# Performance work log

Hardware: AMD Instinct MI355X
Metric: run time of the kernel (lower is better)

## Reference

```python
import jax, jax.numpy as jnp
import numpy as np

MODES1, MODES2 = 32, 32

def fht_matrix(N):
    # Exact linear-operator form of the repo's recursive fht1d (N must be a power of two,
    # which it is here, so the pad/truncate branch never triggers).
    if N == 1:
        return np.ones((1, 1), np.float32)
    M = fht_matrix(N // 2)
    k = np.arange(N // 2)
    cas = (np.cos(2 * np.pi * k / N) + np.sin(2 * np.pi * k / N)).astype(np.float32)[:, None]
    E = np.zeros((N // 2, N), np.float32); E[:, 0::2] = M   # even-index sub-transform
    O = np.zeros((N // 2, N), np.float32); O[:, 1::2] = M   # odd-index sub-transform
    return np.concatenate([E + cas * O, E - cas * O], axis=0)

def dht2(x, M1, M2):
    # apply the (pseudo-)Hartley transform along dims 2 then 3: X[k,l] = sum_{h,w} M1[k,h] M2[l,w] x[h,w]
    return jnp.einsum('bchw,kh,lw->bckl', x, M1, M2)

def neg_freq(a):
    # index map k -> (-k mod m) on the last two dims (flip then roll by 1)
    return jnp.roll(jnp.flip(a, axis=(-2, -1)), shift=(1, 1), axis=(-2, -1))

def compl_mul2d(x1, x2):
    x1n = neg_freq(x1)
    x2n = neg_freq(x2)
    return 0.5 * (jnp.einsum('bixy,ioxy->boxy', x1, x2)
                  - jnp.einsum('bixy,ioxy->boxy', x1n, x2n)
                  + jnp.einsum('bixy,ioxy->boxy', x1, x2n)
                  + jnp.einsum('bixy,ioxy->boxy', x1n, x2))

def setup_inputs() -> dict:
    key = jax.random.key(0)
    k1, k2 = jax.random.split(key)
    B, Cin, Cout, S = 32, 64, 64, 128
    x = jax.random.normal(k1, (B, Cin, S, S), jnp.float32)
    scale = 1.0 / (Cin * Cout)
    weights1 = scale * jax.random.uniform(k2, (Cin, Cout, MODES1, MODES2), jnp.float32)
    return {"x": x, "weights1": weights1}

def reference(x, weights1):
    B, Cin, S1, S2 = x.shape
    Cout = weights1.shape[1]
    M1 = jnp.asarray(fht_matrix(S1))
    M2 = jnp.asarray(fht_matrix(S2))
    x_ht = dht2(x, M1, M2)                                        # [B,Cin,S1,S2]
    block = compl_mul2d(x_ht[:, :, :MODES1, :MODES2], weights1)   # [B,Cout,m1,m2]
    out_ht = jnp.zeros((B, Cout, S1, S2), x.dtype).at[:, :, :MODES1, :MODES2].set(block)
    # idht = dht / (S1*S2)
    return dht2(out_ht, M1, M2) / (S1 * S2)
```

## Files before the change

kernel.cpp:

```cpp
#include <hip/hip_runtime.h>
#include <math.h>


#define SS   128
#define MD   32
#define NBAT 32
#define CI   64
#define CO   64

#define TWO_PI 6.2831853071795864769

typedef __attribute__((ext_vector_type(8))) short bf16x8;
typedef __attribute__((ext_vector_type(4))) float f32x4;

static const size_t OFF_M    = 0;
static const size_t OFF_MT   = 16384;
static const size_t OFF_XH   = 32768;
static const size_t OFF_XHT  = 32768 + 2097152;
static const size_t OFF_WT   = 32768 + 2 * 2097152;
static const size_t OFF_BLKT = OFF_XH;
static const size_t OFF_BLK  = OFF_XHT;
static const size_t OFF_MFH  = OFF_WT + 4194304;
static const size_t OFF_MFL  = OFF_MFH + 2048;

__device__ inline float m_entry(int k, int n) {
    float prod = 1.f;
    int kk = k, nn = n;
    for (int Nj = SS; Nj > 1; Nj >>= 1) {
        int half = Nj >> 1;
        int k1 = kk & (half - 1);
        if (nn & 1) {
            double ang = (TWO_PI / (double)Nj) * (double)k1;
            float cas = (float)(cos(ang) + sin(ang));
            prod *= (kk < half) ? cas : -cas;
        }
        kk = k1;
        nn >>= 1;
    }
    return prod;
}

__device__ inline unsigned short f2bf(float f) {
    unsigned u = __float_as_uint(f);
    return (unsigned short)((u + 0x7FFF + ((u >> 16) & 1)) >> 16);
}
__device__ inline float bf2f(unsigned short h) {
    return __uint_as_float((unsigned)h << 16);
}
__device__ inline void split2(float a, float b, unsigned& hi, unsigned& lo) {
    unsigned short ah = f2bf(a), bh = f2bf(b);
    hi = (unsigned)ah | ((unsigned)bh << 16);
    lo = (unsigned)f2bf(a - bf2f(ah)) | ((unsigned)f2bf(b - bf2f(bh)) << 16);
}

__global__ __launch_bounds__(256) void k_prep(const float* __restrict__ wgt,
                                              float* __restrict__ M,
                                              float* __restrict__ MT,
                                              float* __restrict__ Wt,
                                              unsigned short* __restrict__ MFH,
                                              unsigned short* __restrict__ MFL) {
    const int bid = blockIdx.x;
    const int t   = threadIdx.x;
    if (bid < 64) {
        int idx = bid * 256 + t;
        int k = idx >> 7, n = idx & 127;
        float prod = m_entry(k, n);
        M[idx] = prod;
        MT[n * 128 + k] = prod;
        return;
    }
    if (bid >= 4160) {
        int idx2 = (bid - 4160) * 256 + t;
        int j    = idx2 & 7;
        int lane = (idx2 >> 3) & 63;
        int s    = (idx2 >> 9) & 3;
        int tt   = idx2 >> 11;
        int kq   = tt * 16 + (lane & 15);
        int nq   = s * 32 + ((lane >> 4) << 3) + j;
        float f  = m_entry(kq, nq);
        unsigned short hi = f2bf(f);
        MFH[idx2] = hi;
        MFL[idx2] = f2bf(f - bf2f(hi));
        return;
    }
    __shared__ float tile[32][33];
    const int b2  = bid - 64;
    const int mt  = b2 & 31;
    const int iot = b2 >> 5;
    const int tx = t & 31;
    const int ty = t >> 5;
#pragma unroll
    for (int j = 0; j < 4; ++j) {
        int r = ty + 8 * j;
        tile[r][tx] = wgt[(iot * 32 + r) * 1024 + mt * 32 + tx];
    }
    __syncthreads();
#pragma unroll
    for (int j = 0; j < 4; ++j) {
        int r = ty + 8 * j;
        Wt[(mt * 32 + r) * 4096 + iot * 32 + tx] = tile[tx][r];
    }
}

__global__ __launch_bounds__(256, 3) void k_fwd2(const float* __restrict__ x,
                                                 const unsigned short* __restrict__ MFH,
                                                 const unsigned short* __restrict__ MFL,
                                                 float* __restrict__ Xh) {
    const int bc = blockIdx.x;
    const float* xp = x + (size_t)bc * 16384;
    const int t = threadIdx.x;
    const int lane = t & 63, wid = t >> 6;
    const int l15 = lane & 15, g = lane >> 4;

    __shared__ unsigned short Pan[2][2][4096];
    __shared__ unsigned short Ybf[2][32 * 136];

    const int sh0 = t >> 3, swq = t & 7;

    {
#pragma unroll
        for (int q = 0; q < 4; ++q) {
            int h = sh0 + 32 * q;
            float4 v = *(const float4*)(xp + h * 128 + swq * 4);
            unsigned h01, l01, h23, l23;
            split2(v.x, v.y, h01, l01);
            split2(v.z, v.w, h23, l23);
            int i8 = h * 8 + (swq ^ ((h & 3) << 1));
            ((uint2*)&Pan[0][0][0])[i8] = make_uint2(h01, h23);
            ((uint2*)&Pan[0][1][0])[i8] = make_uint2(l01, l23);
        }
    }

    f32x4 acc[2][2] = {};
    const int hbase = wid * 32;

    for (int s = 0; s < 4; ++s) {
        __syncthreads();
        const int cur = s & 1, nxt = cur ^ 1;
        float4 pre[4];
        if (s < 3) {
#pragma unroll
            for (int q = 0; q < 4; ++q)
                pre[q] = *(const float4*)(xp + (sh0 + 32 * q) * 128 + (s + 1) * 32 + swq * 4);
        }
        bf16x8 Bh[2], Bl[2];
#pragma unroll
        for (int lt = 0; lt < 2; ++lt) {
            int bidx = (lt * 4 + s) * 64 + lane;
            Bh[lt] = ((const bf16x8*)MFH)[bidx];
            Bl[lt] = ((const bf16x8*)MFL)[bidx];
        }
#pragma unroll
        for (int hh = 0; hh < 2; ++hh) {
            int h = hbase + hh * 16 + l15;
            int aidx = h * 4 + (g ^ (h & 3));
            bf16x8 Ah = ((const bf16x8*)&Pan[cur][0][0])[aidx];
            bf16x8 Al = ((const bf16x8*)&Pan[cur][1][0])[aidx];
#pragma unroll
            for (int lt = 0; lt < 2; ++lt) {
                acc[hh][lt] = __builtin_amdgcn_mfma_f32_16x16x32_bf16(Ah, Bh[lt], acc[hh][lt], 0, 0, 0);
                acc[hh][lt] = __builtin_amdgcn_mfma_f32_16x16x32_bf16(Ah, Bl[lt], acc[hh][lt], 0, 0, 0);
                acc[hh][lt] = __builtin_amdgcn_mfma_f32_16x16x32_bf16(Al, Bh[lt], acc[hh][lt], 0, 0, 0);
            }
        }
        if (s < 3) {
#pragma unroll
            for (int q = 0; q < 4; ++q) {
                int h = sh0 + 32 * q;
                unsigned h01, l01, h23, l23;
                split2(pre[q].x, pre[q].y, h01, l01);
                split2(pre[q].z, pre[q].w, h23, l23);
                int i8 = h * 8 + (swq ^ ((h & 3) << 1));
                ((uint2*)&Pan[nxt][0][0])[i8] = make_uint2(h01, h23);
                ((uint2*)&Pan[nxt][1][0])[i8] = make_uint2(l01, l23);
            }
        }
    }

#pragma unroll
    for (int hh = 0; hh < 2; ++hh) {
#pragma unroll
        for (int lt = 0; lt < 2; ++lt) {
            int lmode = lt * 16 + l15;
            int h0 = hbase + hh * 16 + g * 4;
            f32x4 v = acc[hh][lt];
            unsigned hi01, lo01, hi23, lo23;
            split2(v[0], v[1], hi01, lo01);
            split2(v[2], v[3], hi23, lo23);
            ((uint2*)&Ybf[0][0])[lmode * 34 + (h0 >> 2)] = make_uint2(hi01, hi23);
            ((uint2*)&Ybf[1][0])[lmode * 34 + (h0 >> 2)] = make_uint2(lo01, lo23);
        }
    }
    __syncthreads();

    const int kt = wid >> 1, lt2 = wid & 1;
    f32x4 z = {};
#pragma unroll
    for (int s2 = 0; s2 < 4; ++s2) {
        int aidx = (kt * 4 + s2) * 64 + lane;
        bf16x8 Ah = ((const bf16x8*)MFH)[aidx];
        bf16x8 Al = ((const bf16x8*)MFL)[aidx];
        int lmode = lt2 * 16 + l15;
        int yidx = lmode * 17 + s2 * 4 + g;
        bf16x8 Yh = ((const bf16x8*)&Ybf[0][0])[yidx];
        bf16x8 Yl = ((const bf16x8*)&Ybf[1][0])[yidx];
        z = __builtin_amdgcn_mfma_f32_16x16x32_bf16(Ah, Yh, z, 0, 0, 0);
        z = __builtin_amdgcn_mfma_f32_16x16x32_bf16(Ah, Yl, z, 0, 0, 0);
        z = __builtin_amdgcn_mfma_f32_16x16x32_bf16(Al, Yh, z, 0, 0, 0);
    }
    float* op = Xh + (size_t)bc * 1024;
#pragma unroll
    for (int r = 0; r < 4; ++r)
        op[(kt * 16 + g * 4 + r) * 32 + lt2 * 16 + l15] = z[r];
}

__global__ __launch_bounds__(256) void t_xh(const float* __restrict__ Xh,
                                            float* __restrict__ Xh_t) {
    __shared__ float tile[32][33];
    const int i  = blockIdx.x & 63;
    const int mt = blockIdx.x >> 6;
    const int tx = threadIdx.x & 31;
    const int ty = threadIdx.x >> 5;
#pragma unroll
    for (int j = 0; j < 4; ++j) {
        int b = ty + 8 * j;
        tile[b][tx] = Xh[(b * 64 + i) * 1024 + mt * 32 + tx];
    }
    __syncthreads();
#pragma unroll
    for (int j = 0; j < 4; ++j) {
        int row = ty + 8 * j;
        Xh_t[(mt * 32 + row) * 2048 + i * 32 + tx] = tile[tx][row];
    }
}

__global__ __launch_bounds__(256) void k_mix4(const float* __restrict__ Xh_t,
                                              const float* __restrict__ Wt,
                                              float* __restrict__ blk_t) {
    const int m  = blockIdx.x;
    const int xm = m >> 5, ym = m & 31;
    const int nm = (((32 - xm) & 31) << 5) | ((32 - ym) & 31);
    if (m > nm) return;
    const int t = threadIdx.x;

    __shared__ float Xs[2][64][32];

    {
        const float4* xm4 = (const float4*)(Xh_t + m * 2048);
        const float4* xn4 = (const float4*)(Xh_t + nm * 2048);
        float4* s0 = (float4*)&Xs[0][0][0];
        float4* s1 = (float4*)&Xs[1][0][0];
        s0[t]       = xm4[t];
        s0[t + 256] = xm4[t + 256];
        s1[t]       = xn4[t];
        s1[t + 256] = xn4[t + 256];
    }
    __syncthreads();

    const int o  = t & 63;
    const int bq = t >> 6;
    const float* wpm = Wt + m * 4096 + o;
    const float* wpn = Wt + nm * 4096 + o;

    float am[8], an[8];
#pragma unroll
    for (int j = 0; j < 8; ++j) { am[j] = 0.f; an[j] = 0.f; }

#pragma unroll 4
    for (int i = 0; i < 64; ++i) {
        float wm = wpm[i * 64];
        float wn = wpn[i * 64];
        float we = 0.5f * (wm + wn);
        float wo = 0.5f * (wm - wn);
        const float* xr  = &Xs[0][i][bq * 8];
        const float* xrn = &Xs[1][i][bq * 8];
#pragma unroll
        for (int j = 0; j < 8; ++j) {
            float x1  = xr[j];
            float x1n = xrn[j];
            am[j] = fmaf(x1, we, fmaf(x1n, wo, am[j]));
            an[j] = fmaf(x1n, we, fmaf(x1, -wo, an[j]));
        }
    }

    float* om = blk_t + m * 2048 + o;
    float* on = blk_t + nm * 2048 + o;
#pragma unroll
    for (int j = 0; j < 8; ++j) {
        int b = bq * 8 + j;
        om[b * 64] = am[j];
        on[b * 64] = an[j];
    }
}

__global__ __launch_bounds__(256) void t_blk(const float* __restrict__ blk_t,
                                             float* __restrict__ blk) {
    __shared__ float tile[32][33];
    const int mt  = blockIdx.x & 31;
    const int bot = blockIdx.x >> 5;
    const int tx = threadIdx.x & 31;
    const int ty = threadIdx.x >> 5;
#pragma unroll
    for (int j = 0; j < 4; ++j) {
        int r = ty + 8 * j;
        tile[r][tx] = blk_t[(mt * 32 + r) * 2048 + bot * 32 + tx];
    }
    __syncthreads();
#pragma unroll
    for (int j = 0; j < 4; ++j) {
        int r = ty + 8 * j;
        blk[(bot * 32 + r) * 1024 + mt * 32 + tx] = tile[tx][r];
    }
}

__global__ __launch_bounds__(256) void k_inv(const float* __restrict__ blk,
                                             const float* __restrict__ M,
                                             const float* __restrict__ MT,
                                             float* __restrict__ out) {
    const int bo = blockIdx.x;
    const int t  = threadIdx.x;
    __shared__ float smem[8448];
    float* Mcs  = smem;
    float* Ts   = smem + 4224;
    float* outS = smem;

#pragma unroll
    for (int j = 0; j < 16; ++j) {
        int idx = t + j * 256;
        int r = idx >> 5, h = idx & 31;
        Mcs[r * 33 + h] = M[r * 128 + h] * (1.f / 16384.f);
    }
    __syncthreads();

    const int r  = t & 127;
    const int rh = __builtin_amdgcn_readfirstlane(t >> 7);

    {
        const float* bp = blk + (size_t)bo * (MD * MD);
        float acc[16];
#pragma unroll
        for (int j = 0; j < 16; ++j) acc[j] = 0.f;
#pragma unroll 4
        for (int h = 0; h < MD; ++h) {
            float mc = Mcs[r * 33 + h];
            const float* brow = bp + h * MD + rh * 16;
#pragma unroll
            for (int j = 0; j < 16; ++j)
                acc[j] = fmaf(brow[j], mc, acc[j]);
        }
#pragma unroll
        for (int j = 0; j < 16; ++j) Ts[r * 33 + rh * 16 + j] = acc[j];
    }
    __syncthreads();

    float acc[64];
#pragma unroll
    for (int j = 0; j < 64; ++j) acc[j] = 0.f;
#pragma unroll 2
    for (int l = 0; l < MD; ++l) {
        float tv = Ts[r * 33 + l];
        const float* mt = MT + l * 128 + rh * 64;
#pragma unroll
        for (int j = 0; j < 64; ++j)
            acc[j] = fmaf(mt[j], tv, acc[j]);
    }

    float* op = out + (size_t)bo * (SS * SS);
    for (int rr = 0; rr < 2; ++rr) {
        __syncthreads();
        if (rh == rr) {
#pragma unroll
            for (int j = 0; j < 64; ++j) outS[r * 65 + j] = acc[j];
        }
        __syncthreads();
        const int cc = t & 63;
        const int r0 = t >> 6;
#pragma unroll
        for (int j = 0; j < 32; ++j) {
            int rrow = r0 + 4 * j;
            op[rrow * SS + rr * 64 + cc] = outS[rrow * 65 + cc];
        }
    }
}

extern "C" void kernel_launch(void* const* d_in, const int* in_sizes, int n_in,
                              void* d_out, int out_size, void* d_ws, size_t ws_size,
                              hipStream_t stream) {
    const float* x   = (const float*)d_in[0];
    const float* wgt = (const float*)d_in[1];
    float* outp = (float*)d_out;
    float* ws   = (float*)d_ws;

    float* M     = ws + OFF_M;
    float* MT    = ws + OFF_MT;
    float* Xh    = ws + OFF_XH;
    float* Xh_t  = ws + OFF_XHT;
    float* Wt    = ws + OFF_WT;
    float* blk_t = ws + OFF_BLKT;
    float* blk   = ws + OFF_BLK;
    unsigned short* MFH = (unsigned short*)(ws + OFF_MFH);
    unsigned short* MFL = (unsigned short*)(ws + OFF_MFL);

    k_prep <<<4176, 256, 0, stream>>>(wgt, M, MT, Wt, MFH, MFL);
    k_fwd2 <<<2048, 256, 0, stream>>>(x, MFH, MFL, Xh);
    t_xh   <<<2048, 256, 0, stream>>>(Xh, Xh_t);
    k_mix4 <<<1024, 256, 0, stream>>>(Xh_t, Wt, blk_t);
    t_blk  <<<2048, 256, 0, stream>>>(blk_t, blk);
    k_inv  <<<2048, 256, 0, stream>>>(blk, M, MT, outp);
}
```

Measured before the change: 122.4 us.

## Rewrite inverse Hartley transform with split-bf16 MFMA and drop fp32 matrix prep

Replaces the scalar-FMA inverse transform kernel with one that runs both separable matrix products on bf16 MFMA instructions. It uses hi/lo bf16 splitting and three MFMAs per tile to keep near-fp32 accuracy. The intermediate is staged in LDS as split bf16, and results are written with float4 stores. The fp32 M/MT precompute in the prep kernel is removed, and the inverse now reuses the packed MFH/MFL fragments also used by the forward kernel. This cuts FMA and VGPR pressure in the largest output-writing kernel, at the cost of extra rounding from the bf16 split.

```diff
diff --git a/kernel.cpp b/kernel.cpp
--- a/kernel.cpp
+++ b/kernel.cpp
@@ -13,15 +13,13 @@
 typedef __attribute__((ext_vector_type(8))) short bf16x8;
 typedef __attribute__((ext_vector_type(4))) float f32x4;
 
-static const size_t OFF_M    = 0;
-static const size_t OFF_MT   = 16384;
 static const size_t OFF_XH   = 32768;
 static const size_t OFF_XHT  = 32768 + 2097152;
 static const size_t OFF_WT   = 32768 + 2 * 2097152;
 static const size_t OFF_BLKT = OFF_XH;
 static const size_t OFF_BLK  = OFF_XHT;
 static const size_t OFF_MFH  = OFF_WT + 4194304;
-static const size_t OFF_MFL  = OFF_MFH + 2048;
+static const size_t OFF_MFL  = OFF_MFH + 8192;
 
 __device__ inline float m_entry(int k, int n) {
     float prod = 1.f;
@@ -54,23 +52,13 @@
 }
 
 __global__ __launch_bounds__(256) void k_prep(const float* __restrict__ wgt,
-                                              float* __restrict__ M,
-                                              float* __restrict__ MT,
                                               float* __restrict__ Wt,
                                               unsigned short* __restrict__ MFH,
                                               unsigned short* __restrict__ MFL) {
     const int bid = blockIdx.x;
     const int t   = threadIdx.x;
-    if (bid < 64) {
-        int idx = bid * 256 + t;
-        int k = idx >> 7, n = idx & 127;
-        float prod = m_entry(k, n);
-        M[idx] = prod;
-        MT[n * 128 + k] = prod;
-        return;
-    }
-    if (bid >= 4160) {
-        int idx2 = (bid - 4160) * 256 + t;
+    if (bid >= 4096) {
+        int idx2 = (bid - 4096) * 256 + t;
         int j    = idx2 & 7;
         int lane = (idx2 >> 3) & 63;
         int s    = (idx2 >> 9) & 3;
@@ -84,9 +72,8 @@
         return;
     }
     __shared__ float tile[32][33];
-    const int b2  = bid - 64;
-    const int mt  = b2 & 31;
-    const int iot = b2 >> 5;
+    const int mt  = bid & 31;
+    const int iot = bid >> 5;
     const int tx = t & 31;
     const int ty = t >> 5;
 #pragma unroll
@@ -313,72 +300,76 @@
     }
 }
 
-__global__ __launch_bounds__(256) void k_inv(const float* __restrict__ blk,
-                                             const float* __restrict__ M,
-                                             const float* __restrict__ MT,
-                                             float* __restrict__ out) {
+__global__ __launch_bounds__(256, 2) void k_inv2(const float* __restrict__ blk,
+                                                 const unsigned short* __restrict__ MFH,
+                                                 const unsigned short* __restrict__ MFL,
+                                                 float* __restrict__ out) {
     const int bo = blockIdx.x;
     const int t  = threadIdx.x;
-    __shared__ float smem[8448];
-    float* Mcs  = smem;
-    float* Ts   = smem + 4224;
-    float* outS = smem;
-
-#pragma unroll
-    for (int j = 0; j < 16; ++j) {
-        int idx = t + j * 256;
-        int r = idx >> 5, h = idx & 31;
-        Mcs[r * 33 + h] = M[r * 128 + h] * (1.f / 16384.f);
-    }
-    __syncthreads();
-
-    const int r  = t & 127;
-    const int rh = __builtin_amdgcn_readfirstlane(t >> 7);
+    const int lane = t & 63, wid = t >> 6;
+    const int l15 = lane & 15, g = lane >> 4;
+
+    __shared__ __align__(16) unsigned short Bst[2][32 * 40];
+    __shared__ __align__(16) unsigned short Tl[2][128 * 40];
 
     {
-        const float* bp = blk + (size_t)bo * (MD * MD);
-        float acc[16];
-#pragma unroll
-        for (int j = 0; j < 16; ++j) acc[j] = 0.f;
-#pragma unroll 4
-        for (int h = 0; h < MD; ++h) {
-            float mc = Mcs[r * 33 + h];
-            const float* brow = bp + h * MD + rh * 16;
-#pragma unroll
-            for (int j = 0; j < 16; ++j)
-                acc[j] = fmaf(brow[j], mc, acc[j]);
-        }
-#pragma unroll
-        for (int j = 0; j < 16; ++j) Ts[r * 33 + rh * 16 + j] = acc[j];
-    }
-    __syncthreads();
-
-    float acc[64];
-#pragma unroll
-    for (int j = 0; j < 64; ++j) acc[j] = 0.f;
-#pragma unroll 2
-    for (int l = 0; l < MD; ++l) {
-        float tv = Ts[r * 33 + l];
-        const float* mt = MT + l * 128 + rh * 64;
-#pragma unroll
-        for (int j = 0; j < 64; ++j)
-            acc[j] = fmaf(mt[j], tv, acc[j]);
-    }
+        float4 v = ((const float4*)(blk + (size_t)bo * 1024))[t];
+        const int h = t >> 3, l0 = (t & 7) * 4;
+        float vv[4] = { v.x * (1.f / 16384.f), v.y * (1.f / 16384.f),
+                        v.z * (1.f / 16384.f), v.w * (1.f / 16384.f) };
+#pragma unroll
+        for (int q = 0; q < 4; ++q) {
+            unsigned short hi = f2bf(vv[q]);
+            Bst[0][(l0 + q) * 40 + h] = hi;
+            Bst[1][(l0 + q) * 40 + h] = f2bf(vv[q] - bf2f(hi));
+        }
+    }
+    __syncthreads();
+
+#pragma unroll
+    for (int rr = 0; rr < 2; ++rr) {
+        const int tt = wid * 2 + rr;
+        const int aidx = (tt * 4) * 64 + lane;
+        bf16x8 Ah = ((const bf16x8*)MFH)[aidx];
+        bf16x8 Al = ((const bf16x8*)MFL)[aidx];
+#pragma unroll
+        for (int lt = 0; lt < 2; ++lt) {
+            bf16x8 Bh = *(const bf16x8*)&Bst[0][(lt * 16 + l15) * 40 + g * 8];
+            bf16x8 Bl = *(const bf16x8*)&Bst[1][(lt * 16 + l15) * 40 + g * 8];
+            f32x4 acc = {};
+            acc = __builtin_amdgcn_mfma_f32_16x16x32_bf16(Ah, Bh, acc, 0, 0, 0);
+            acc = __builtin_amdgcn_mfma_f32_16x16x32_bf16(Al, Bh, acc, 0, 0, 0);
+            acc = __builtin_amdgcn_mfma_f32_16x16x32_bf16(Ah, Bl, acc, 0, 0, 0);
+#pragma unroll
+            for (int ri = 0; ri < 4; ++ri) {
+                int r = tt * 16 + g * 4 + ri;
+                int l = lt * 16 + l15;
+                unsigned short hi = f2bf(acc[ri]);
+                Tl[0][r * 40 + l] = hi;
+                Tl[1][r * 40 + l] = f2bf(acc[ri] - bf2f(hi));
+            }
+        }
+    }
+    __syncthreads();
 
     float* op = out + (size_t)bo * (SS * SS);
+#pragma unroll
     for (int rr = 0; rr < 2; ++rr) {
-        __syncthreads();
-        if (rh == rr) {
-#pragma unroll
-            for (int j = 0; j < 64; ++j) outS[r * 65 + j] = acc[j];
-        }
-        __syncthreads();
-        const int cc = t & 63;
-        const int r0 = t >> 6;
-#pragma unroll
-        for (int j = 0; j < 32; ++j) {
-            int rrow = r0 + 4 * j;
-            op[rrow * SS + rr * 64 + cc] = outS[rrow * 65 + cc];
+        const int rt = wid * 2 + rr;
+        bf16x8 Bh = *(const bf16x8*)&Tl[0][(rt * 16 + l15) * 40 + g * 8];
+        bf16x8 Bl = *(const bf16x8*)&Tl[1][(rt * 16 + l15) * 40 + g * 8];
+        const int r = rt * 16 + l15;
+#pragma unroll
+        for (int ct = 0; ct < 8; ++ct) {
+            const int aidx = (ct * 4) * 64 + lane;
+            bf16x8 Ah = ((const bf16x8*)MFH)[aidx];
+            bf16x8 Al = ((const bf16x8*)MFL)[aidx];
+            f32x4 acc = {};
+            acc = __builtin_amdgcn_mfma_f32_16x16x32_bf16(Ah, Bh, acc, 0, 0, 0);
+            acc = __builtin_amdgcn_mfma_f32_16x16x32_bf16(Al, Bh, acc, 0, 0, 0);
+            acc = __builtin_amdgcn_mfma_f32_16x16x32_bf16(Ah, Bl, acc, 0, 0, 0);
+            *(float4*)&op[r * SS + ct * 16 + g * 4] =
+                make_float4(acc[0], acc[1], acc[2], acc[3]);
         }
     }
 }
@@ -391,8 +382,6 @@
     float* outp = (float*)d_out;
     float* ws   = (float*)d_ws;
 
-    float* M     = ws + OFF_M;
-    float* MT    = ws + OFF_MT;
     float* Xh    = ws + OFF_XH;
     float* Xh_t  = ws + OFF_XHT;
     float* Wt    = ws + OFF_WT;
@@ -401,10 +390,10 @@
     unsigned short* MFH = (unsigned short*)(ws + OFF_MFH);
     unsigned short* MFL = (unsigned short*)(ws + OFF_MFL);
 
-    k_prep <<<4176, 256, 0, stream>>>(wgt, M, MT, Wt, MFH, MFL);
+    k_prep <<<4160, 256, 0, stream>>>(wgt, Wt, MFH, MFL);
     k_fwd2 <<<2048, 256, 0, stream>>>(x, MFH, MFL, Xh);
     t_xh   <<<2048, 256, 0, stream>>>(Xh, Xh_t);
     k_mix4 <<<1024, 256, 0, stream>>>(Xh_t, Wt, blk_t);
     t_blk  <<<2048, 256, 0, stream>>>(blk_t, blk);
-    k_inv  <<<2048, 256, 0, stream>>>(blk, M, MT, outp);
-}
+    k_inv2 <<<2048, 256, 0, stream>>>(blk, MFH, MFL, outp);
+}
```

Measured after the change: 108.2 us. -11.6%, faster.
